# Optimization experiments

Hardware: AMD Instinct MI355X
Metric: run time of the kernel (lower is better)

Reference implementation:

```python
import jax, jax.numpy as jnp
import numpy as np

B, S, D, H = 4, 1024, 1024, 16
DH = D // H  # head dim = 64


def setup_inputs() -> dict:
    key = jax.random.key(0)
    k0, k1, k2 = jax.random.split(key, 3)
    x = jax.random.normal(k0, (B, S, D), dtype=jnp.float32)
    c_attn_w = jax.random.normal(k1, (D, 3 * D), dtype=jnp.float32) * 0.02
    c_attn_b = jnp.zeros((3 * D,), dtype=jnp.float32)
    c_proj_w = jax.random.normal(k2, (D, D), dtype=jnp.float32) * 0.02
    c_proj_b = jnp.zeros((D,), dtype=jnp.float32)
    return {"x": x, "c_attn_w": c_attn_w, "c_attn_b": c_attn_b,
            "c_proj_w": c_proj_w, "c_proj_b": c_proj_b}


def reference(x, c_attn_w, c_attn_b, c_proj_w, c_proj_b):
    b, s, d = x.shape
    # Conv1D (GPT-2 style): out = x @ W + b, fused QKV
    qkv = jnp.einsum('bsd,de->bse', x, c_attn_w) + c_attn_b
    q, k, v = jnp.split(qkv, 3, axis=-1)
    # split heads -> [b, h, s, dh]
    q = q.reshape(b, s, H, DH).transpose(0, 2, 1, 3)
    k = k.reshape(b, s, H, DH).transpose(0, 2, 1, 3)
    v = v.reshape(b, s, H, DH).transpose(0, 2, 1, 3)
    # scaled scores with causal future mask (triu above diagonal -> -inf)
    w = jnp.einsum('bhqd,bhkd->bhqk', q, k) / jnp.sqrt(jnp.asarray(DH, x.dtype))
    future = jnp.triu(jnp.ones((s, s), dtype=bool), k=1)
    w = jnp.where(future[None, None, :, :], jnp.asarray(-jnp.inf, w.dtype), w)
    p = jax.nn.softmax(w, axis=-1)
    a = jnp.einsum('bhqk,bhkd->bhqd', p, v)
    # merge heads -> [b, s, d]
    a = a.transpose(0, 2, 1, 3).reshape(b, s, d)
    # output projection (Conv1D)
    out = jnp.einsum('bsd,de->bse', a, c_proj_w) + c_proj_b
    return out
```

## Files before the change

kernel.cpp:

```cpp
#include <hip/hip_runtime.h>
#include <math.h>

#define BB 4
#define SS 1024
#define DD 1024
#define HH 16
#define DHH 64

typedef short bf16x8 __attribute__((ext_vector_type(8)));
typedef float f32x4 __attribute__((ext_vector_type(4)));

__device__ __forceinline__ unsigned short f2bf(float f) {
    unsigned u = __float_as_uint(f);
    u += 0x7fffu + ((u >> 16) & 1u);
    return (unsigned short)(u >> 16);
}

__device__ __forceinline__ void glds16(const void* g, void* l) {
    __builtin_amdgcn_global_load_lds(
        (const __attribute__((address_space(1))) unsigned int*)g,
        (__attribute__((address_space(3))) unsigned int*)l, 16, 0, 0);
}

#define WAITCNT_VM(n)  (0xF70 | (n))
#define WAITCNT_LGKM0  (0xC07F)

__device__ __forceinline__ int swz(int row, int col) {
    return ((((col >> 4) ^ (row >> 2)) & 3) << 4) | (col & 15);
}

__global__ __launch_bounds__(256) void prologue_kernel(
    const float* __restrict__ x, const float* __restrict__ w1,
    const float* __restrict__ w2, unsigned short* __restrict__ Xb,
    unsigned short* __restrict__ W1t, unsigned short* __restrict__ W2t)
{
    __shared__ float tile[64][65];
    const int bx = blockIdx.x;
    if (bx < 4096) {
        int i = bx * 256 + threadIdx.x;
        float4 v = ((const float4*)x)[i];
        ushort4 o = { f2bf(v.x), f2bf(v.y), f2bf(v.z), f2bf(v.w) };
        ((ushort4*)Xb)[i] = o;
        return;
    }
    const float* W; unsigned short* Wt; int N, n0, k0;
    if (bx < 4864) {
        int id = bx - 4096; W = w1; Wt = W1t; N = 3072;
        n0 = (id % 48) * 64; k0 = (id / 48) * 64;
    } else {
        int id = bx - 4864; W = w2; Wt = W2t; N = 1024;
        n0 = (id & 15) * 64; k0 = (id >> 4) * 64;
    }
    int c = threadIdx.x & 63, r0 = threadIdx.x >> 6;
    #pragma unroll
    for (int i = 0; i < 16; ++i) {
        int r = r0 + i * 4;
        tile[r][c] = W[(size_t)(k0 + r) * N + n0 + c];
    }
    __syncthreads();
    #pragma unroll
    for (int i = 0; i < 16; ++i) {
        int r = r0 + i * 4;
        Wt[(size_t)(n0 + r) * 1024 + k0 + c] = f2bf(tile[c][r]);
    }
}

__global__ __launch_bounds__(512, 2) void gemm_mfma(
    const unsigned short* __restrict__ A,
    const unsigned short* __restrict__ Bt,
    const float* __restrict__ bias,
    unsigned short* __restrict__ Cout,
    unsigned short* __restrict__ Vt,
    int N, int K)
{
    __shared__ unsigned short smem[65536];

    const int t = threadIdx.x;
    const int lane = t & 63;
    const int w = t >> 6;
    const int l15 = lane & 15, quad = lane >> 4;
    const int wr = w >> 2, wc = w & 3;
    const int bm = blockIdx.y * 256, bn = blockIdx.x * 256;

    const int sl_ca = ((lane & 7) ^ (lane >> 3)) << 4;
    const unsigned short* sl_base =
        (sl_ca < 64) ? (A + (size_t)bm * K) : (Bt + (size_t)bn * K);
    const int sl_k = (sl_ca & 63) >> 1;

    auto stage = [&](int tile, int kh, int rh) {
        #pragma unroll
        for (int j = 0; j < 2; ++j) {
            int row = rh * 128 + j * 64 + w * 8 + (lane >> 3);
            glds16(sl_base + (size_t)row * K + tile * 64 + kh * 32 + sl_k,
                   &smem[((tile & 1) * 2 + kh) * 16384 +
                         rh * 8192 + j * 4096 + w * 512]);
        }
    };

    const f32x4 zero4 = {0.f, 0.f, 0.f, 0.f};
    f32x4 acc[8][4];
    #pragma unroll
    for (int i = 0; i < 8; ++i)
        #pragma unroll
        for (int j = 0; j < 4; ++j) acc[i][j] = zero4;

    const int T = K / 64;

    stage(0, 0, 0); stage(0, 0, 1); stage(0, 1, 0); stage(0, 1, 1);
    stage(1, 0, 0); stage(1, 0, 1);
    __builtin_amdgcn_s_waitcnt(WAITCNT_VM(4));

    bf16x8 bfr[4];
    for (int tt = 0; tt < T; ++tt) {
        const int buf = tt & 1;
        #pragma unroll
        for (int ph = 0; ph < 4; ++ph) {
            const int kh = ph >> 1;
            const int mh = ph & 1;
            __builtin_amdgcn_s_barrier();
            __builtin_amdgcn_sched_barrier(0);

            bf16x8 af[4];
            #pragma unroll
            for (int i = 0; i < 4; ++i) {
                int row = wr * 128 + (mh * 4 + i) * 16 + l15;
                int byte = (row << 7) + (quad << 4);
                byte ^= (l15 & 7) << 4;
                af[i] = *(const bf16x8*)&smem[(buf * 2 + kh) * 16384 + (byte >> 1)];
            }
            if (mh == 0) {
                #pragma unroll
                for (int nj = 0; nj < 4; ++nj) {
                    int row = wc * 64 + nj * 16 + l15;
                    int byte = (row << 7) + 64 + (quad << 4);
                    byte ^= (l15 & 7) << 4;
                    bfr[nj] = *(const bf16x8*)&smem[(buf * 2 + kh) * 16384 + (byte >> 1)];
                }
            }

            if (ph == 0)      { if (tt + 1 < T) stage(tt + 1, 1, 0); }
            else if (ph == 1) { if (tt + 1 < T) stage(tt + 1, 1, 1); }
            else if (ph == 2) { if (tt + 2 < T) stage(tt + 2, 0, 0); }
            else              { if (tt + 2 < T) stage(tt + 2, 0, 1); }

            __builtin_amdgcn_s_setprio(1);
            #pragma unroll
            for (int i = 0; i < 4; ++i)
                #pragma unroll
                for (int nj = 0; nj < 4; ++nj)
                    acc[mh * 4 + i][nj] = __builtin_amdgcn_mfma_f32_16x16x32_bf16(
                        af[i], bfr[nj], acc[mh * 4 + i][nj], 0, 0, 0);
            __builtin_amdgcn_s_setprio(0);
        }
        if (tt + 2 < T)      __builtin_amdgcn_s_waitcnt(WAITCNT_VM(4));
        else if (tt + 1 < T) __builtin_amdgcn_s_waitcnt(WAITCNT_VM(0));
    }

    __syncthreads();

    float bv[4];
    #pragma unroll
    for (int nj = 0; nj < 4; ++nj) bv[nj] = bias[bn + wc * 64 + nj * 16 + l15];

    if (bn >= 2048) {
        #pragma unroll
        for (int mi = 0; mi < 8; ++mi)
            #pragma unroll
            for (int nj = 0; nj < 4; ++nj)
                #pragma unroll
                for (int r = 0; r < 4; ++r) {
                    int row = wr * 128 + mi * 16 + quad * 4 + r;
                    int col = wc * 64 + nj * 16 + l15;
                    smem[col * 256 + (row ^ (((col >> 2) & 3) << 4))] =
                        f2bf(acc[mi][nj][r] + bv[nj]);
                }
        __syncthreads();
        int b = bm >> 10, s0 = bm & 1023;
        int h0 = (bn - 2048) >> 6;
        #pragma unroll
        for (int it = 0; it < 16; ++it) {
            int chunk = it * 512 + t;
            int col = chunk >> 5;
            int r8 = (chunk & 31) * 8;
            bf16x8 val = *(const bf16x8*)&smem[col * 256 +
                         (r8 ^ (((col >> 2) & 3) << 4))];
            int h = h0 + (col >> 6), dh = col & 63;
            *(bf16x8*)&Vt[(((size_t)b * 16 + h) * 64 + dh) * 1024 + s0 + r8] = val;
        }
    } else {
        #pragma unroll
        for (int mi = 0; mi < 8; ++mi)
            #pragma unroll
            for (int nj = 0; nj < 4; ++nj)
                #pragma unroll
                for (int r = 0; r < 4; ++r) {
                    int row = wr * 128 + mi * 16 + quad * 4 + r;
                    int col = wc * 64 + nj * 16 + l15;
                    smem[row * 256 + (col ^ (((row >> 2) & 3) << 4))] =
                        f2bf(acc[mi][nj][r] + bv[nj]);
                }
        __syncthreads();
        #pragma unroll
        for (int it = 0; it < 16; ++it) {
            int chunk = it * 512 + t;
            int row = chunk >> 5;
            int col = (chunk & 31) * 8;
            bf16x8 val = *(const bf16x8*)&smem[row * 256 +
                         (col ^ (((row >> 2) & 3) << 4))];
            *(bf16x8*)&Cout[(size_t)(bm + row) * N + bn + col] = val;
        }
    }
}

__global__ __launch_bounds__(256) void gemm2_mfma(
    const unsigned short* __restrict__ A,
    const unsigned short* __restrict__ Bt,
    const float* __restrict__ bias,
    float* __restrict__ C,
    int N, int K)
{
    __shared__ unsigned short smem[18432];

    const int t = threadIdx.x;
    const int lane = t & 63;
    const int w = t >> 6;
    const int l15 = lane & 15, quad = lane >> 4;
    const int bm = blockIdx.y * 64, bn = blockIdx.x * 128;

    const int fragoff = l15 * K + quad * 8;

    const f32x4 zero4 = {0.f, 0.f, 0.f, 0.f};
    f32x4 acc[2][4];
    #pragma unroll
    for (int i = 0; i < 2; ++i)
        #pragma unroll
        for (int j = 0; j < 4; ++j) acc[i][j] = zero4;

    const unsigned short* Abase = A  + (size_t)bm * K + fragoff;
    const unsigned short* Bbase = Bt + (size_t)bn * K + fragoff;

    const int R = K / 32;

    auto issue = [&](int k, int b) {
        glds16(Abase + (size_t)(w * 16) * K + k * 32,
               &smem[b * 6144 + w * 512]);
        #pragma unroll
        for (int g2 = 0; g2 < 2; ++g2) {
            int g = w * 2 + g2;
            glds16(Bbase + (size_t)(g * 16) * K + k * 32,
                   &smem[b * 6144 + 2048 + g * 512]);
        }
    };

    issue(0, 0);
    issue(1, 1);
    for (int k = 0; k < R; ++k) {
        if (k + 2 < R) {
            issue(k + 2, (k + 2) % 3);
            __builtin_amdgcn_s_waitcnt(WAITCNT_VM(6));
        } else if (k + 1 < R) {
            __builtin_amdgcn_s_waitcnt(WAITCNT_VM(3));
        } else {
            __builtin_amdgcn_s_waitcnt(WAITCNT_VM(0));
        }
        __builtin_amdgcn_s_barrier();

        bf16x8 af[2], bfr[4];
        #pragma unroll
        for (int mi = 0; mi < 2; ++mi)
            af[mi] = *(const bf16x8*)&smem[(k % 3) * 6144 + ((w >> 1) * 2 + mi) * 512 + lane * 8];
        #pragma unroll
        for (int nj = 0; nj < 4; ++nj)
            bfr[nj] = *(const bf16x8*)&smem[(k % 3) * 6144 + 2048 + ((w & 1) * 4 + nj) * 512 + lane * 8];
        #pragma unroll
        for (int mi = 0; mi < 2; ++mi)
            #pragma unroll
            for (int nj = 0; nj < 4; ++nj)
                acc[mi][nj] = __builtin_amdgcn_mfma_f32_16x16x32_bf16(
                    af[mi], bfr[nj], acc[mi][nj], 0, 0, 0);

        __builtin_amdgcn_s_barrier();
    }

    const int wm = (w >> 1) * 32;
    const int wn = (w & 1) * 64;
    float bv[4];
    #pragma unroll
    for (int nj = 0; nj < 4; ++nj) bv[nj] = bias[bn + wn + nj * 16 + l15];

    float* fs = (float*)smem;
    #pragma unroll
    for (int mi = 0; mi < 2; ++mi)
        #pragma unroll
        for (int nj = 0; nj < 4; ++nj)
            #pragma unroll
            for (int r = 0; r < 4; ++r)
                fs[(wm + mi * 16 + quad * 4 + r) * 128 + wn + nj * 16 + l15] =
                    acc[mi][nj][r] + bv[nj];
    __syncthreads();
    #pragma unroll
    for (int i = 0; i < 8; ++i) {
        int off = i * 256 + t;
        int row = off >> 5, col = (off & 31) * 4;
        *(float4*)&C[(size_t)(bm + row) * N + bn + col] =
            *(const float4*)&fs[row * 128 + col];
    }
}

__device__ __forceinline__ void attn_tile_step8(
    bf16x8 q0, bf16x8 q1, float* lsum, f32x4* o,
    const unsigned short (*Ks)[80], const unsigned short (*VsT)[80],
    unsigned short (*Ps)[80],
    int wq, int l15, int quad, bool diag)
{
    const f32x4 zero4 = {0.f, 0.f, 0.f, 0.f};
    f32x4 s[4];
    #pragma unroll
    for (int nj = 0; nj < 4; ++nj) {
        int n = nj * 16 + l15;
        f32x4 sa = zero4;
        bf16x8 b0 = *(const bf16x8*)&Ks[n][swz(n, quad * 8)];
        bf16x8 b1 = *(const bf16x8*)&Ks[n][swz(n, 32 + quad * 8)];
        sa = __builtin_amdgcn_mfma_f32_16x16x32_bf16(q0, b0, sa, 0, 0, 0);
        sa = __builtin_amdgcn_mfma_f32_16x16x32_bf16(q1, b1, sa, 0, 0, 0);
        s[nj] = sa;
    }
    const float scale = 0.125f;

    #pragma unroll
    for (int nj = 0; nj < 4; ++nj)
        #pragma unroll
        for (int r = 0; r < 4; ++r) {
            float sv = s[nj][r] * scale;
            if (diag && (nj * 16 + l15) > (wq * 16 + quad * 4 + r)) sv = -INFINITY;
            float p = __expf(sv);
            lsum[r] += p;
            int qloc = wq * 16 + quad * 4 + r;
            Ps[qloc][swz(qloc, nj * 16 + l15)] = f2bf(p);
        }

    #pragma unroll
    for (int kk = 0; kk < 2; ++kk) {
        int m = wq * 16 + l15;
        bf16x8 pa = *(const bf16x8*)&Ps[m][swz(m, kk * 32 + quad * 8)];
        #pragma unroll
        for (int nj = 0; nj < 4; ++nj) {
            int n = nj * 16 + l15;
            bf16x8 vb = *(const bf16x8*)&VsT[n][swz(n, kk * 32 + quad * 8)];
            o[nj] = __builtin_amdgcn_mfma_f32_16x16x32_bf16(pa, vb, o[nj], 0, 0, 0);
        }
    }
}

__global__ __launch_bounds__(512) void attn_mfma(
    const unsigned short* __restrict__ qkv,
    const unsigned short* __restrict__ Vt,
    unsigned short* __restrict__ aout)
{
    __shared__ unsigned short Ks[64][80];
    __shared__ unsigned short VsT[64][80];
    __shared__ unsigned short Ps[2][64][80];

    const int t = threadIdx.x;
    const int lane = t & 63;
    const int wave = t >> 6;
    const int wq = wave & 3;
    const int tile = wave >> 2;
    const int l15 = lane & 15, quad = lane >> 4;
    const int qlo = blockIdx.x;
    const int qhi = 15 - qlo;
    const int qb = tile ? qhi : qlo;
    const int bh = blockIdx.y;
    const int b = bh >> 4, h = bh & 15;
    const size_t qkvbase = (size_t)b * SS * 3072;
    const f32x4 zero4 = {0.f, 0.f, 0.f, 0.f};

    bf16x8 qf0, qf1;
    {
        const unsigned short* p = qkv + qkvbase +
            (size_t)(qb * 64 + wq * 16 + l15) * 3072 + h * 64 + quad * 8;
        qf0 = *(const bf16x8*)p;
        qf1 = *(const bf16x8*)(p + 32);
    }

    float lsum[4];
    f32x4 o[4];
    #pragma unroll
    for (int r = 0; r < 4; ++r) lsum[r] = 0.f;
    #pragma unroll
    for (int nj = 0; nj < 4; ++nj) o[nj] = zero4;

    const int sr = t >> 3, scc = (t & 7) * 8;
    const unsigned short* kgp = qkv + qkvbase + 1024 + h * 64 + (size_t)sr * 3072 + scc;
    const unsigned short* vgp = Vt + ((size_t)bh * 64 + sr) * 1024 + scc;
    bf16x8 kreg, vreg;

    kreg = *(const bf16x8*)(kgp);
    vreg = *(const bf16x8*)(vgp);

    for (int kb = 0; kb <= qhi; ++kb) {
        __builtin_amdgcn_s_barrier();
        *(bf16x8*)&Ks[sr][swz(sr, scc)] = kreg;
        *(bf16x8*)&VsT[sr][swz(sr, scc)] = vreg;
        if (kb < qhi) {
            kreg = *(const bf16x8*)(kgp + (size_t)(kb + 1) * 64 * 3072);
            vreg = *(const bf16x8*)(vgp + (kb + 1) * 64);
        }
        __builtin_amdgcn_s_waitcnt(WAITCNT_LGKM0);
        __builtin_amdgcn_s_barrier();

        if (kb <= qb)
            attn_tile_step8(qf0, qf1, lsum, o, Ks, VsT, Ps[tile],
                            wq, l15, quad, kb == qb);
    }

    #pragma unroll
    for (int off = 1; off < 16; off <<= 1)
        #pragma unroll
        for (int r = 0; r < 4; ++r)
            lsum[r] += __shfl_xor(lsum[r], off);

    #pragma unroll
    for (int r = 0; r < 4; ++r) {
        float inv = 1.0f / lsum[r];
        int rloc = wq * 16 + quad * 4 + r;
        size_t ob = ((size_t)b * SS + qb * 64 + rloc) * 1024 + h * 64;
        #pragma unroll
        for (int nj = 0; nj < 4; ++nj)
            aout[ob + nj * 16 + l15] = f2bf(o[nj][r] * inv);
    }
}

extern "C" void kernel_launch(void* const* d_in, const int* in_sizes, int n_in,
                              void* d_out, int out_size, void* d_ws, size_t ws_size,
                              hipStream_t stream)
{
    const float* x     = (const float*)d_in[0];
    const float* wqkv  = (const float*)d_in[1];
    const float* bqkv  = (const float*)d_in[2];
    const float* wproj = (const float*)d_in[3];
    const float* bproj = (const float*)d_in[4];
    float* out = (float*)d_out;

    unsigned short* ws   = (unsigned short*)d_ws;
    unsigned short* Xb   = ws;
    unsigned short* W1t  = Xb  + (size_t)4096 * 1024;
    unsigned short* W2t  = W1t + (size_t)3072 * 1024;
    unsigned short* qkv  = W2t + (size_t)1024 * 1024;
    unsigned short* Vt   = qkv + (size_t)4096 * 3072;
    unsigned short* abuf = Vt  + (size_t)64 * 64 * 1024;

    prologue_kernel<<<5120, 256, 0, stream>>>(x, wqkv, wproj, Xb, W1t, W2t);

    gemm_mfma<<<dim3(3072 / 256, 4096 / 256), 512, 0, stream>>>(
        Xb, W1t, bqkv, qkv, Vt, 3072, 1024);

    attn_mfma<<<dim3(8, 64), 512, 0, stream>>>(qkv, Vt, abuf);

    gemm2_mfma<<<dim3(1024 / 128, 4096 / 64), 256, 0, stream>>>(
        abuf, W2t, bproj, out, 1024, 1024);
}
```

Measured before the change: 167.8 us.

## Double-buffer GEMM register fragments to overlap LDS reads with MFMA

Restructures the QKV GEMM main loop so the LDS fragments for the next phase are loaded into a second register set while the current phase's MFMAs run. The barrier moves to the end of each phase, and the global-load wait is shifted to phase 2 with a tighter count. The goal is to hide LDS read latency behind matrix math. In exchange it uses more VGPRs for the doubled fragments, and the reordered wait/barrier placement must stay correct against the asynchronous global->LDS staging.

Result: no change. 169.3 us (+0.9%).

```diff
diff --git a/kernel.cpp b/kernel.cpp
--- a/kernel.cpp
+++ b/kernel.cpp
@@ -97,6 +97,25 @@
         }
     };
 
+    auto rd_af = [&](bf16x8* dst, int buf, int kh, int mh) {
+        #pragma unroll
+        for (int i = 0; i < 4; ++i) {
+            int row = wr * 128 + (mh * 4 + i) * 16 + l15;
+            int byte = (row << 7) + (quad << 4);
+            byte ^= (l15 & 7) << 4;
+            dst[i] = *(const bf16x8*)&smem[(buf * 2 + kh) * 16384 + (byte >> 1)];
+        }
+    };
+    auto rd_bf = [&](bf16x8* dst, int buf, int kh) {
+        #pragma unroll
+        for (int nj = 0; nj < 4; ++nj) {
+            int row = wc * 64 + nj * 16 + l15;
+            int byte = (row << 7) + 64 + (quad << 4);
+            byte ^= (l15 & 7) << 4;
+            dst[nj] = *(const bf16x8*)&smem[(buf * 2 + kh) * 16384 + (byte >> 1)];
+        }
+    };
+
     const f32x4 zero4 = {0.f, 0.f, 0.f, 0.f};
     f32x4 acc[8][4];
     #pragma unroll
@@ -105,43 +124,36 @@
         for (int j = 0; j < 4; ++j) acc[i][j] = zero4;
 
     const int T = K / 64;
+
+    bf16x8 afr[2][4], bfr[2][4];
 
     stage(0, 0, 0); stage(0, 0, 1); stage(0, 1, 0); stage(0, 1, 1);
     stage(1, 0, 0); stage(1, 0, 1);
     __builtin_amdgcn_s_waitcnt(WAITCNT_VM(4));
-
-    bf16x8 bfr[4];
+    __builtin_amdgcn_s_barrier();
+    __builtin_amdgcn_sched_barrier(0);
+    rd_af(afr[0], 0, 0, 0);
+    rd_bf(bfr[0], 0, 0);
+    __builtin_amdgcn_sched_barrier(0);
+
     for (int tt = 0; tt < T; ++tt) {
         const int buf = tt & 1;
         #pragma unroll
         for (int ph = 0; ph < 4; ++ph) {
-            const int kh = ph >> 1;
             const int mh = ph & 1;
-            __builtin_amdgcn_s_barrier();
-            __builtin_amdgcn_sched_barrier(0);
-
-            bf16x8 af[4];
-            #pragma unroll
-            for (int i = 0; i < 4; ++i) {
-                int row = wr * 128 + (mh * 4 + i) * 16 + l15;
-                int byte = (row << 7) + (quad << 4);
-                byte ^= (l15 & 7) << 4;
-                af[i] = *(const bf16x8*)&smem[(buf * 2 + kh) * 16384 + (byte >> 1)];
-            }
-            if (mh == 0) {
-                #pragma unroll
-                for (int nj = 0; nj < 4; ++nj) {
-                    int row = wc * 64 + nj * 16 + l15;
-                    int byte = (row << 7) + 64 + (quad << 4);
-                    byte ^= (l15 & 7) << 4;
-                    bfr[nj] = *(const bf16x8*)&smem[(buf * 2 + kh) * 16384 + (byte >> 1)];
-                }
-            }
 
             if (ph == 0)      { if (tt + 1 < T) stage(tt + 1, 1, 0); }
             else if (ph == 1) { if (tt + 1 < T) stage(tt + 1, 1, 1); }
             else if (ph == 2) { if (tt + 2 < T) stage(tt + 2, 0, 0); }
             else              { if (tt + 2 < T) stage(tt + 2, 0, 1); }
+
+            if (ph == 0)      { rd_af(afr[1], buf, 0, 1); }
+            else if (ph == 1) { rd_af(afr[0], buf, 1, 0); rd_bf(bfr[1], buf, 1); }
+            else if (ph == 2) { rd_af(afr[1], buf, 1, 1); }
+            else if (tt + 1 < T) {
+                rd_af(afr[0], buf ^ 1, 0, 0); rd_bf(bfr[0], buf ^ 1, 0);
+            }
+            __builtin_amdgcn_sched_barrier(0);
 
             __builtin_amdgcn_s_setprio(1);
             #pragma unroll
@@ -149,11 +161,17 @@
                 #pragma unroll
                 for (int nj = 0; nj < 4; ++nj)
                     acc[mh * 4 + i][nj] = __builtin_amdgcn_mfma_f32_16x16x32_bf16(
-                        af[i], bfr[nj], acc[mh * 4 + i][nj], 0, 0, 0);
+                        afr[ph & 1][i], bfr[ph >> 1][nj], acc[mh * 4 + i][nj], 0, 0, 0);
             __builtin_amdgcn_s_setprio(0);
-        }
-        if (tt + 2 < T)      __builtin_amdgcn_s_waitcnt(WAITCNT_VM(4));
-        else if (tt + 1 < T) __builtin_amdgcn_s_waitcnt(WAITCNT_VM(0));
+            __builtin_amdgcn_sched_barrier(0);
+
+            if (ph == 2) {
+                if (tt + 2 < T) __builtin_amdgcn_s_waitcnt(WAITCNT_VM(2));
+                else            __builtin_amdgcn_s_waitcnt(WAITCNT_VM(0));
+            }
+            __builtin_amdgcn_s_barrier();
+            __builtin_amdgcn_sched_barrier(0);
+        }
     }
 
     __syncthreads();
```
